# Kernel optimization log

Hardware: AMD Instinct MI355X
Metric: run time of the kernel (lower is better)

## Reference

```python
import jax, jax.numpy as jnp
import numpy as np

EPS = 1e-7  # K.epsilon()

def squash(s, axis=-1):
    # v = (||s||^2 / (1 + ||s||^2)) * s / ||s||
    sq = jnp.sum(jnp.square(s), axis=axis, keepdims=True)
    scale = sq / (1.0 + sq) / jnp.sqrt(sq + EPS)
    return scale * s

def setup_inputs() -> dict:
    key = jax.random.key(0)
    k1, k2, k3 = jax.random.split(key, 3)
    B, J, P = 128, 2048, 8      # batch, input_num_capsule, input_dim_capsule
    N, D = 32, 16               # num_capsule, dim_capsule
    x = jax.random.normal(k1, (B, J, P), dtype=jnp.float32)
    W = jax.random.normal(k2, (N, J, D, P), dtype=jnp.float32) * 0.1
    bias = jax.random.normal(k3, (N, D), dtype=jnp.float32) * 0.1
    return {"x": x, "W": W, "bias": bias}

def reference(x, W, bias):
    # x: [B, J, P], W: [N, J, D, P], bias: [N, D]
    routings = 3
    # inputs_hat[b,n,j,d] = sum_p W[n,j,d,p] * x[b,j,p]   -> [B, N, J, D]
    u_hat = jnp.einsum('njdp,bjp->bnjd', W, x)
    B_, N, J, _ = u_hat.shape
    b = jnp.zeros((B_, N, J), dtype=u_hat.dtype)
    outputs = None
    for i in range(routings):
        c = jax.nn.softmax(b, axis=1)                      # coupling over output caps
        s = jnp.einsum('bnj,bnjd->bnd', c, u_hat) + bias   # weighted sum + bias
        outputs = squash(s)                                # [B, N, D]
        if i < routings - 1:
            b = b + jnp.einsum('bnd,bnjd->bnj', outputs, u_hat)  # agreement
    return outputs
```

## Files before the change

kernel.cpp:

```cpp
#include <hip/hip_runtime.h>
#include <hip/hip_bf16.h>

#define B_   128
#define J_   2048
#define N_   32
#define D_   16
#define NJC  32

typedef __attribute__((ext_vector_type(8))) short short8b;
typedef __attribute__((ext_vector_type(4))) float f32x4;
typedef __attribute__((ext_vector_type(16))) float f32x16;

__device__ inline short bf16s(float f) {
    union { __hip_bfloat16 h; short s; } u;
    u.h = __float2bfloat16(f);
    return u.s;
}


__global__ __launch_bounds__(256) void capsT(const float* __restrict__ x,
                                             float* __restrict__ xT) {
    __shared__ float tile[32 * 260 + 4];
    const int t  = threadIdx.x;
    const int jt = blockIdx.x & 63;
    const int bt = blockIdx.x >> 6;
    const int j0 = jt * 32, b0 = bt * 32;

    for (int idx = t; idx < 2048; idx += 256) {
        int bl = idx >> 6, f4 = idx & 63;
        float4 v = *(const float4*)(x + (size_t)(b0 + bl) * 16384 + j0 * 8 + f4 * 4);
        *(float4*)&tile[bl * 260 + f4 * 4] = v;
    }
    __syncthreads();
    for (int idx = t; idx < 2048; idx += 256) {
        int jj = idx >> 6, f4o = idx & 63;
        int bl = f4o >> 1, po = (f4o & 1) * 4;
        float4 v = *(const float4*)&tile[bl * 260 + jj * 8 + po];
        *(float4*)(xT + ((size_t)(j0 + jj) * 128 + b0 + bl) * 8 + po) = v;
    }
}

__global__ __launch_bounds__(256) void capsA(const float* __restrict__ W,
                                             const float* __restrict__ xT,
                                             const __hip_bfloat16* __restrict__ blogT,
                                             const float2* __restrict__ mdT,
                                             float* __restrict__ s_part,
                                             int mode) {
    const int t     = threadIdx.x;
    const int lane  = t & 63;
    const int i     = blockIdx.x;
    const int jc    = (i & 7) + 8 * (i >> 8);
    const int n     = (i >> 3) & 31;
    const int wv    = t >> 6;
    const int colid = lane & 15;
    const int kgrp  = lane >> 4;

    const int b0 = wv * 32 + colid;
    const int b1 = b0 + 16;

    f32x4 acc0 = {0.f, 0.f, 0.f, 0.f};
    f32x4 acc1 = {0.f, 0.f, 0.f, 0.f};

    for (int ks = 0; ks < 16; ++ks) {
        const int j = jc * 64 + ks * 4 + kgrp;

        const float4* wp = (const float4*)(W + (((size_t)n * J_ + j) * 16 + colid) * 8);
        float4 wa = wp[0], wb = wp[1];
        short8b bfrag;
        bfrag[0] = bf16s(wa.x); bfrag[1] = bf16s(wa.y);
        bfrag[2] = bf16s(wa.z); bfrag[3] = bf16s(wa.w);
        bfrag[4] = bf16s(wb.x); bfrag[5] = bf16s(wb.y);
        bfrag[6] = bf16s(wb.z); bfrag[7] = bf16s(wb.w);

        float c0 = 1.0f / 32.0f, c1 = 1.0f / 32.0f;
        if (mode) {
            float lg0 = __bfloat162float(blogT[((size_t)n * J_ + j) * B_ + b0]);
            float lg1 = __bfloat162float(blogT[((size_t)n * J_ + j) * B_ + b1]);
            float2 m0 = mdT[(size_t)j * B_ + b0];
            float2 m1 = mdT[(size_t)j * B_ + b1];
            c0 = __expf(lg0 - m0.x) * m0.y;
            c1 = __expf(lg1 - m1.x) * m1.y;
        }

        const float4* xp0 = (const float4*)(xT + ((size_t)j * 128 + b0) * 8);
        float4 xa = xp0[0], xb = xp0[1];
        short8b afrag0;
        afrag0[0] = bf16s(xa.x * c0); afrag0[1] = bf16s(xa.y * c0);
        afrag0[2] = bf16s(xa.z * c0); afrag0[3] = bf16s(xa.w * c0);
        afrag0[4] = bf16s(xb.x * c0); afrag0[5] = bf16s(xb.y * c0);
        afrag0[6] = bf16s(xb.z * c0); afrag0[7] = bf16s(xb.w * c0);

        const float4* xp1 = (const float4*)(xT + ((size_t)j * 128 + b1) * 8);
        float4 xe = xp1[0], xf = xp1[1];
        short8b afrag1;
        afrag1[0] = bf16s(xe.x * c1); afrag1[1] = bf16s(xe.y * c1);
        afrag1[2] = bf16s(xe.z * c1); afrag1[3] = bf16s(xe.w * c1);
        afrag1[4] = bf16s(xf.x * c1); afrag1[5] = bf16s(xf.y * c1);
        afrag1[6] = bf16s(xf.z * c1); afrag1[7] = bf16s(xf.w * c1);

        acc0 = __builtin_amdgcn_mfma_f32_16x16x32_bf16(afrag0, bfrag, acc0, 0, 0, 0);
        acc1 = __builtin_amdgcn_mfma_f32_16x16x32_bf16(afrag1, bfrag, acc1, 0, 0, 0);
    }

    float* sdst = s_part + (size_t)jc * (B_ * N_ * D_);
    #pragma unroll
    for (int r = 0; r < 4; ++r) {
        int brow = wv * 32 + kgrp * 4 + r;
        sdst[(size_t)brow * 512 + n * 16 + colid]        = acc0[r];
        sdst[(size_t)(brow + 16) * 512 + n * 16 + colid] = acc1[r];
    }
}

__global__ __launch_bounds__(256) void capsR(const float* __restrict__ s_part,
                                             const float* __restrict__ bias,
                                             float* __restrict__ out,
                                             __hip_bfloat16* __restrict__ oT) {
    int gid = blockIdx.x * 256 + threadIdx.x;
    float sv = bias[gid & 511];
    #pragma unroll
    for (int jc = 0; jc < NJC; ++jc)
        sv += s_part[(size_t)jc * 65536 + gid];
    float sq = sv * sv;
    sq += __shfl_xor(sq, 1);
    sq += __shfl_xor(sq, 2);
    sq += __shfl_xor(sq, 4);
    sq += __shfl_xor(sq, 8);
    float scale = sq / (1.0f + sq) / sqrtf(sq + 1e-7f);
    float ov = scale * sv;
    out[gid] = ov;
    int b = gid >> 9, nd = gid & 511;
    int n = nd >> 4, d = nd & 15;
    oT[((size_t)n * B_ + b) * D_ + d] = __float2bfloat16(ov);
}

__global__ __launch_bounds__(256) void capsB(const float* __restrict__ W,
                                             const float* __restrict__ xT,
                                             const __hip_bfloat16* __restrict__ oT,
                                             __hip_bfloat16* __restrict__ blogT,
                                             int accumulate) {
    __shared__ float w_lds[16 * 544];
    const int t    = threadIdx.x;
    const int lane = t & 63;
    const int i    = blockIdx.x;
    const int xcd  = i & 7;
    const int r    = i >> 3;
    const int jq   = xcd * 64 + (r & 63);
    const int nh   = r >> 6;
    const int j0   = jq * 4;
    const int wv   = t >> 6;
    const int g    = lane >> 5;
    const int col  = lane & 31;
    const int jl   = col >> 3;
    const int p    = col & 7;
    const int bt   = wv;

    #pragma unroll
    for (int q = 0; q < 8; ++q) {
        int f = t + q * 256;
        int n_idx = f >> 7;
        int rem = f & 127;
        int row = rem >> 5, c4 = rem & 31;
        float4 v = *(const float4*)(W + ((size_t)(nh * 16 + n_idx) * J_ + j0 + row) * 128 + c4 * 4);
        *(float4*)&w_lds[n_idx * 544 + row * 136 + c4 * 4] = v;
    }
    __syncthreads();

    float4 xv[4];
    #pragma unroll
    for (int jl2 = 0; jl2 < 4; ++jl2)
        xv[jl2] = *(const float4*)(xT + ((size_t)(j0 + jl2) * 128 + bt * 32 + col) * 8 + g * 4);

    f32x16 zz;
    #pragma unroll
    for (int q = 0; q < 16; ++q) zz[q] = 0.0f;

    for (int nn = 0; nn < 16; ++nn) {
        const int n = nh * 16 + nn;

        short8b bfrag = *(const short8b*)(oT + ((size_t)n * B_ + bt * 32 + col) * D_ + g * 8);

        const float* wrow = &w_lds[nn * 544 + jl * 136 + g * 64 + p];
        short8b afrag;
        #pragma unroll
        for (int q = 0; q < 8; ++q)
            afrag[q] = bf16s(wrow[q * 8]);

        f32x16 acc =
            __builtin_amdgcn_mfma_f32_32x32x16_bf16(afrag, bfrag, zz, 0, 0, 0);

        const int b = bt * 32 + col;
        #pragma unroll
        for (int jl2 = 0; jl2 < 4; ++jl2) {
            const int j = j0 + jl2;
            float4 v = xv[jl2];
            float tt = acc[jl2 * 4 + 0] * v.x
                     + acc[jl2 * 4 + 1] * v.y
                     + acc[jl2 * 4 + 2] * v.z
                     + acc[jl2 * 4 + 3] * v.w;
            tt += __shfl_xor(tt, 32);
            if (g == (jl2 >> 1)) {
                size_t a0 = ((size_t)n * J_ + j) * B_ + b;
                if (accumulate) tt += __bfloat162float(blogT[a0]);
                blogT[a0] = __float2bfloat16(tt);
            }
        }
    }
}

__global__ __launch_bounds__(256) void capsD(const __hip_bfloat16* __restrict__ blogT,
                                             float2* __restrict__ mdT) {
    int gid = blockIdx.x * 256 + threadIdx.x;
    float v[32];
    float m = -1e30f;
    #pragma unroll
    for (int nn = 0; nn < 32; ++nn) {
        v[nn] = __bfloat162float(blogT[(size_t)nn * (J_ * B_) + gid]);
        m = fmaxf(m, v[nn]);
    }
    float sum = 0.0f;
    #pragma unroll
    for (int nn = 0; nn < 32; ++nn) sum += __expf(v[nn] - m);
    mdT[gid] = make_float2(m, 1.0f / sum);
}

extern "C" void kernel_launch(void* const* d_in, const int* in_sizes, int n_in,
                              void* d_out, int out_size, void* d_ws, size_t ws_size,
                              hipStream_t stream) {
    const float* x    = (const float*)d_in[0];
    const float* W    = (const float*)d_in[1];
    const float* bias = (const float*)d_in[2];
    float* out = (float*)d_out;

    float* ws = (float*)d_ws;
    float*           xT     = ws;
    __hip_bfloat16*  blogT  = (__hip_bfloat16*)(ws + 2097152);
    float2*          mdT    = (float2*)(ws + 2097152 + 4194304);
    float*           s_part = ws + 2097152 + 4194304 + 524288;
    __hip_bfloat16*  oT     = (__hip_bfloat16*)(ws + 8912896);

    dim3 b256(256);

    capsT<<<dim3(256), b256, 0, stream>>>(x, xT);

    capsA<<<dim3(1024), b256, 0, stream>>>(W, xT, blogT, mdT, s_part, 0);
    capsR<<<dim3(256), b256, 0, stream>>>(s_part, bias, out, oT);
    capsB<<<dim3(1024), b256, 0, stream>>>(W, xT, oT, blogT, 0);

    capsD<<<dim3(1024), b256, 0, stream>>>(blogT, mdT);
    capsA<<<dim3(1024), b256, 0, stream>>>(W, xT, blogT, mdT, s_part, 1);
    capsR<<<dim3(256), b256, 0, stream>>>(s_part, bias, out, oT);
    capsB<<<dim3(1024), b256, 0, stream>>>(W, xT, oT, blogT, 1);

    capsD<<<dim3(1024), b256, 0, stream>>>(blogT, mdT);
    capsA<<<dim3(1024), b256, 0, stream>>>(W, xT, blogT, mdT, s_part, 1);
    capsR<<<dim3(256), b256, 0, stream>>>(s_part, bias, out, oT);
}
```

Before: 144.7 us.

## Pre-convert W to bf16 copies and precompute softmax coefficients in capsD

Adds a prep kernel that converts W once into a bf16 copy and a transposed bf16 copy laid out for the capsB MFMA operand. capsA and capsB then read bf16 weights directly, which halves weight traffic in the five passes, and capsB drops its LDS staging and barrier. capsD now writes normalized bf16 coupling coefficients, so capsA loads them instead of recomputing the exponentials. The cost is an extra pass over W, a larger workspace, and a coefficient write as large as the logit tensor.

```diff
diff --git a/kernel.cpp b/kernel.cpp
--- a/kernel.cpp
+++ b/kernel.cpp
@@ -17,6 +17,35 @@
     return u.s;
 }
 
+
+__global__ __launch_bounds__(256) void capsW(const float* __restrict__ W,
+                                             __hip_bfloat16* __restrict__ Wbf,
+                                             __hip_bfloat16* __restrict__ Wt) {
+    __shared__ float lds[16 * 132];
+    const int t = threadIdx.x;
+    const size_t base = (size_t)blockIdx.x * 2048;
+    const int r  = t >> 4;
+    const int e0 = (t & 15) * 8;
+
+    float4 a = *(const float4*)(W + base + t * 8);
+    float4 b = *(const float4*)(W + base + t * 8 + 4);
+    short8b w8;
+    w8[0]=bf16s(a.x); w8[1]=bf16s(a.y); w8[2]=bf16s(a.z); w8[3]=bf16s(a.w);
+    w8[4]=bf16s(b.x); w8[5]=bf16s(b.y); w8[6]=bf16s(b.z); w8[7]=bf16s(b.w);
+    *(short8b*)((short*)Wbf + base + t * 8) = w8;
+    *(float4*)&lds[r * 132 + e0]     = a;
+    *(float4*)&lds[r * 132 + e0 + 4] = b;
+    __syncthreads();
+
+    short8b o8;
+    #pragma unroll
+    for (int k = 0; k < 8; ++k) {
+        int q = e0 + k;
+        int p = q >> 4, d = q & 15;
+        o8[k] = bf16s(lds[r * 132 + d * 8 + p]);
+    }
+    *(short8b*)((short*)Wt + base + t * 8) = o8;
+}
 
 __global__ __launch_bounds__(256) void capsT(const float* __restrict__ x,
                                              float* __restrict__ xT) {
@@ -40,10 +69,9 @@
     }
 }
 
-__global__ __launch_bounds__(256) void capsA(const float* __restrict__ W,
+__global__ __launch_bounds__(256) void capsA(const __hip_bfloat16* __restrict__ Wbf,
                                              const float* __restrict__ xT,
-                                             const __hip_bfloat16* __restrict__ blogT,
-                                             const float2* __restrict__ mdT,
+                                             const __hip_bfloat16* __restrict__ cT,
                                              float* __restrict__ s_part,
                                              int mode) {
     const int t     = threadIdx.x;
@@ -64,22 +92,13 @@
     for (int ks = 0; ks < 16; ++ks) {
         const int j = jc * 64 + ks * 4 + kgrp;
 
-        const float4* wp = (const float4*)(W + (((size_t)n * J_ + j) * 16 + colid) * 8);
-        float4 wa = wp[0], wb = wp[1];
-        short8b bfrag;
-        bfrag[0] = bf16s(wa.x); bfrag[1] = bf16s(wa.y);
-        bfrag[2] = bf16s(wa.z); bfrag[3] = bf16s(wa.w);
-        bfrag[4] = bf16s(wb.x); bfrag[5] = bf16s(wb.y);
-        bfrag[6] = bf16s(wb.z); bfrag[7] = bf16s(wb.w);
+        short8b bfrag = *(const short8b*)((const short*)Wbf
+                          + (((size_t)n * J_ + j) * 16 + colid) * 8);
 
         float c0 = 1.0f / 32.0f, c1 = 1.0f / 32.0f;
         if (mode) {
-            float lg0 = __bfloat162float(blogT[((size_t)n * J_ + j) * B_ + b0]);
-            float lg1 = __bfloat162float(blogT[((size_t)n * J_ + j) * B_ + b1]);
-            float2 m0 = mdT[(size_t)j * B_ + b0];
-            float2 m1 = mdT[(size_t)j * B_ + b1];
-            c0 = __expf(lg0 - m0.x) * m0.y;
-            c1 = __expf(lg1 - m1.x) * m1.y;
+            c0 = __bfloat162float(cT[((size_t)n * J_ + j) * B_ + b0]);
+            c1 = __bfloat162float(cT[((size_t)n * J_ + j) * B_ + b1]);
         }
 
         const float4* xp0 = (const float4*)(xT + ((size_t)j * 128 + b0) * 8);
@@ -133,12 +152,11 @@
     oT[((size_t)n * B_ + b) * D_ + d] = __float2bfloat16(ov);
 }
 
-__global__ __launch_bounds__(256) void capsB(const float* __restrict__ W,
+__global__ __launch_bounds__(256) void capsB(const __hip_bfloat16* __restrict__ Wt,
                                              const float* __restrict__ xT,
                                              const __hip_bfloat16* __restrict__ oT,
                                              __hip_bfloat16* __restrict__ blogT,
                                              int accumulate) {
-    __shared__ float w_lds[16 * 544];
     const int t    = threadIdx.x;
     const int lane = t & 63;
     const int i    = blockIdx.x;
@@ -154,17 +172,6 @@
     const int p    = col & 7;
     const int bt   = wv;
 
-    #pragma unroll
-    for (int q = 0; q < 8; ++q) {
-        int f = t + q * 256;
-        int n_idx = f >> 7;
-        int rem = f & 127;
-        int row = rem >> 5, c4 = rem & 31;
-        float4 v = *(const float4*)(W + ((size_t)(nh * 16 + n_idx) * J_ + j0 + row) * 128 + c4 * 4);
-        *(float4*)&w_lds[n_idx * 544 + row * 136 + c4 * 4] = v;
-    }
-    __syncthreads();
-
     float4 xv[4];
     #pragma unroll
     for (int jl2 = 0; jl2 < 4; ++jl2)
@@ -174,16 +181,14 @@
     #pragma unroll
     for (int q = 0; q < 16; ++q) zz[q] = 0.0f;
 
+    #pragma unroll 2
     for (int nn = 0; nn < 16; ++nn) {
         const int n = nh * 16 + nn;
 
         short8b bfrag = *(const short8b*)(oT + ((size_t)n * B_ + bt * 32 + col) * D_ + g * 8);
 
-        const float* wrow = &w_lds[nn * 544 + jl * 136 + g * 64 + p];
-        short8b afrag;
-        #pragma unroll
-        for (int q = 0; q < 8; ++q)
-            afrag[q] = bf16s(wrow[q * 8]);
+        short8b afrag = *(const short8b*)((const short*)Wt
+                          + (((size_t)n * J_ + j0 + jl) * 8 + p) * 16 + g * 8);
 
         f32x16 acc =
             __builtin_amdgcn_mfma_f32_32x32x16_bf16(afrag, bfrag, zz, 0, 0, 0);
@@ -208,7 +213,7 @@
 }
 
 __global__ __launch_bounds__(256) void capsD(const __hip_bfloat16* __restrict__ blogT,
-                                             float2* __restrict__ mdT) {
+                                             __hip_bfloat16* __restrict__ cT) {
     int gid = blockIdx.x * 256 + threadIdx.x;
     float v[32];
     float m = -1e30f;
@@ -220,7 +225,10 @@
     float sum = 0.0f;
     #pragma unroll
     for (int nn = 0; nn < 32; ++nn) sum += __expf(v[nn] - m);
-    mdT[gid] = make_float2(m, 1.0f / sum);
+    float inv = 1.0f / sum;
+    #pragma unroll
+    for (int nn = 0; nn < 32; ++nn)
+        cT[(size_t)nn * (J_ * B_) + gid] = __float2bfloat16(__expf(v[nn] - m) * inv);
 }
 
 extern "C" void kernel_launch(void* const* d_in, const int* in_sizes, int n_in,
@@ -234,24 +242,27 @@
     float* ws = (float*)d_ws;
     float*           xT     = ws;
     __hip_bfloat16*  blogT  = (__hip_bfloat16*)(ws + 2097152);
-    float2*          mdT    = (float2*)(ws + 2097152 + 4194304);
-    float*           s_part = ws + 2097152 + 4194304 + 524288;
-    __hip_bfloat16*  oT     = (__hip_bfloat16*)(ws + 8912896);
+    __hip_bfloat16*  cT     = (__hip_bfloat16*)(ws + 6291456);
+    float*           s_part = ws + 10485760;
+    __hip_bfloat16*  oT     = (__hip_bfloat16*)(ws + 12582912);
+    __hip_bfloat16*  Wbf    = (__hip_bfloat16*)(ws + 12615680);
+    __hip_bfloat16*  Wt     = (__hip_bfloat16*)(ws + 16809984);
 
     dim3 b256(256);
 
-    capsT<<<dim3(256), b256, 0, stream>>>(x, xT);
-
-    capsA<<<dim3(1024), b256, 0, stream>>>(W, xT, blogT, mdT, s_part, 0);
-    capsR<<<dim3(256), b256, 0, stream>>>(s_part, bias, out, oT);
-    capsB<<<dim3(1024), b256, 0, stream>>>(W, xT, oT, blogT, 0);
-
-    capsD<<<dim3(1024), b256, 0, stream>>>(blogT, mdT);
-    capsA<<<dim3(1024), b256, 0, stream>>>(W, xT, blogT, mdT, s_part, 1);
-    capsR<<<dim3(256), b256, 0, stream>>>(s_part, bias, out, oT);
-    capsB<<<dim3(1024), b256, 0, stream>>>(W, xT, oT, blogT, 1);
-
-    capsD<<<dim3(1024), b256, 0, stream>>>(blogT, mdT);
-    capsA<<<dim3(1024), b256, 0, stream>>>(W, xT, blogT, mdT, s_part, 1);
-    capsR<<<dim3(256), b256, 0, stream>>>(s_part, bias, out, oT);
-}
+    capsW<<<dim3(4096), b256, 0, stream>>>(W, Wbf, Wt);
+    capsT<<<dim3(256),  b256, 0, stream>>>(x, xT);
+
+    capsA<<<dim3(1024), b256, 0, stream>>>(Wbf, xT, cT, s_part, 0);
+    capsR<<<dim3(256),  b256, 0, stream>>>(s_part, bias, out, oT);
+    capsB<<<dim3(1024), b256, 0, stream>>>(Wt, xT, oT, blogT, 0);
+
+    capsD<<<dim3(1024), b256, 0, stream>>>(blogT, cT);
+    capsA<<<dim3(1024), b256, 0, stream>>>(Wbf, xT, cT, s_part, 1);
+    capsR<<<dim3(256),  b256, 0, stream>>>(s_part, bias, out, oT);
+    capsB<<<dim3(1024), b256, 0, stream>>>(Wt, xT, oT, blogT, 1);
+
+    capsD<<<dim3(1024), b256, 0, stream>>>(blogT, cT);
+    capsA<<<dim3(1024), b256, 0, stream>>>(Wbf, xT, cT, s_part, 1);
+    capsR<<<dim3(256),  b256, 0, stream>>>(s_part, bias, out, oT);
+}
```

After: 141.2 us. 1.02x faster.
